# Kernel tuning notes

Hardware: AMD Instinct MI355X
Metric: run time of the kernel (lower is better)

The kernel has to match this reference:

```python
import jax, jax.numpy as jnp
import numpy as np
from jax import lax

EMB = 200   # embedding_dim (GRU hidden size)
SD = 12     # state_dim
AD = 4      # action_dim
CD = 8      # context_dim
LCD = 6     # local_context_dim
T = 100     # rollout steps
BS = 2048   # batch size
EPS = 0.01 ** 2


def _lin(x, w, b):
    # torch nn.Linear convention: y = x @ W^T + b
    return x @ w.T + b


def setup_inputs() -> dict:
    key = jax.random.key(0)
    ks = iter(jax.random.split(key, 64))

    def p(shape):
        return jax.random.normal(next(ks), shape, jnp.float32) * 0.05

    d = {}
    d["x"] = jax.random.normal(next(ks), (BS, SD), jnp.float32)
    d["u"] = jax.random.normal(next(ks), (T, BS, AD), jnp.float32)
    d["ctx_mean"] = jax.random.normal(next(ks), (BS, CD), jnp.float32)
    d["local_ctx"] = jax.random.normal(next(ks), (T, BS, LCD), jnp.float32)
    # state_embed_net: Lin(SD,200) ReLU, Lin(200,EMB) Tanh
    d["se_w1"], d["se_b1"] = p((200, SD)), p((200,))
    d["se_w2"], d["se_b2"] = p((EMB, 200)), p((EMB,))
    # action_embed_net: Lin(AD,200) ReLU, Lin(200,EMB) ReLU
    d["ae_w1"], d["ae_b1"] = p((200, AD)), p((200,))
    d["ae_w2"], d["ae_b2"] = p((EMB, 200)), p((EMB,))
    # context_embed_net: Lin(CD,200) ReLU, Lin(200,EMB) ReLU
    d["ce_w1"], d["ce_b1"] = p((200, CD)), p((200,))
    d["ce_w2"], d["ce_b2"] = p((EMB, 200)), p((EMB,))
    # local_context_embed_net: Lin(LCD,200) ReLU, Lin(200,EMB) ReLU
    d["lce_w1"], d["lce_b1"] = p((200, LCD)), p((200,))
    d["lce_w2"], d["lce_b2"] = p((EMB, 200)), p((EMB,))
    # decode_net: Lin(EMB,200) ReLU, Lin(200,SD)
    d["dec_w1"], d["dec_b1"] = p((200, EMB)), p((200,))
    d["dec_w2"], d["dec_b2"] = p((SD, 200)), p((SD,))
    # GRUCell(input=3*EMB, hidden=EMB)
    d["gru_wih"], d["gru_bih"] = p((3 * EMB, 3 * EMB)), p((3 * EMB,))
    d["gru_whh"], d["gru_bhh"] = p((3 * EMB, EMB)), p((3 * EMB,))
    # hidden_cov_net: Lin(EMB,200) ReLU, Lin(200,SD)
    d["cov_w1"], d["cov_b1"] = p((200, EMB)), p((200,))
    d["cov_w2"], d["cov_b2"] = p((SD, 200)), p((SD,))
    return d


def _forward(x, u, ctx_mean, local_ctx,
             se_w1, se_b1, se_w2, se_b2,
             ae_w1, ae_b1, ae_w2, ae_b2,
             ce_w1, ce_b1, ce_w2, ce_b2,
             lce_w1, lce_b1, lce_w2, lce_b2,
             dec_w1, dec_b1, dec_w2, dec_b2,
             gru_wih, gru_bih, gru_whh, gru_bhh,
             cov_w1, cov_b1, cov_w2, cov_b2):
    relu = jax.nn.relu
    # embeddings (vectorized over all timesteps at once)
    state_embed = jnp.tanh(_lin(relu(_lin(x, se_w1, se_b1)), se_w2, se_b2))          # [BS, EMB]
    action_embed_all = relu(_lin(relu(_lin(u, ae_w1, ae_b1)), ae_w2, ae_b2))         # [T, BS, EMB]
    ctx_embed = relu(_lin(relu(_lin(ctx_mean, ce_w1, ce_b1)), ce_w2, ce_b2))         # [BS, EMB]
    lce_all = relu(_lin(relu(_lin(local_ctx, lce_w1, lce_b1)), lce_w2, lce_b2))      # [T, BS, EMB]

    def step(h, inp):
        a, lc = inp
        gru_in = jnp.concatenate([ctx_embed, a, lc], axis=-1)   # [BS, 3*EMB]
        gi = gru_in @ gru_wih.T + gru_bih                        # [BS, 3*EMB]
        gh = h @ gru_whh.T + gru_bhh                             # [BS, 3*EMB]
        ir, iz, inn = jnp.split(gi, 3, axis=-1)
        hr, hz, hn = jnp.split(gh, 3, axis=-1)
        r = jax.nn.sigmoid(ir + hr)
        z = jax.nn.sigmoid(iz + hz)
        n = jnp.tanh(inn + r * hn)
        h_new = (1.0 - z) * n + z * h
        return h_new, h_new

    _, hs = lax.scan(step, state_embed, (action_embed_all, lce_all))
    hiddens = jnp.concatenate([state_embed[None], hs], axis=0)   # [T+1, BS, EMB]

    state_mean = _lin(relu(_lin(hiddens, dec_w1, dec_b1)), dec_w2, dec_b2)           # [T+1, BS, SD]
    cov = jax.nn.softplus(_lin(relu(_lin(hiddens, cov_w1, cov_b1)), cov_w2, cov_b2)) + EPS
    state_std = jnp.sqrt(cov)                                                        # [T+1, BS, SD]
    return state_mean, state_std


def reference(x, u, ctx_mean, local_ctx,
              se_w1, se_b1, se_w2, se_b2,
              ae_w1, ae_b1, ae_w2, ae_b2,
              ce_w1, ce_b1, ce_w2, ce_b2,
              lce_w1, lce_b1, lce_w2, lce_b2,
              dec_w1, dec_b1, dec_w2, dec_b2,
              gru_wih, gru_bih, gru_whh, gru_bhh,
              cov_w1, cov_b1, cov_w2, cov_b2):
    return _forward(x, u, ctx_mean, local_ctx,
                    se_w1, se_b1, se_w2, se_b2,
                    ae_w1, ae_b1, ae_w2, ae_b2,
                    ce_w1, ce_b1, ce_w2, ce_b2,
                    lce_w1, lce_b1, lce_w2, lce_b2,
                    dec_w1, dec_b1, dec_w2, dec_b2,
                    gru_wih, gru_bih, gru_whh, gru_bhh,
                    cov_w1, cov_b1, cov_w2, cov_b2)
```

## Files before the change

kernel.cpp:

```cpp
#include <hip/hip_runtime.h>
#include <math.h>

#define TT   100
#define BSZ  2048
#define NCH  4
#define CT   (TT/NCH)
#define CR   (CT*BSZ)
#define DR   ((TT+1)*BSZ)
#define NG   624
#define GO   208
#define EPSV 1e-4f

typedef short bfrag __attribute__((ext_vector_type(8)));
typedef float facc  __attribute__((ext_vector_type(4)));

static __device__ __forceinline__ short f2b(float x){
  union { float f; unsigned u; } c; c.f = x;
  unsigned r = (c.u + 0x7FFFu + ((c.u >> 16) & 1u)) >> 16;
  return (short)r;
}
static __device__ __forceinline__ float b2f(short s){
  union { unsigned u; float f; } c; c.u = ((unsigned)(unsigned short)s) << 16;
  return c.f;
}
static __device__ __forceinline__ facc mfma16(bfrag a, bfrag b, facc c){
  return __builtin_amdgcn_mfma_f32_16x16x32_bf16(a, b, c, 0, 0, 0);
}
static __device__ __forceinline__ float sigm(float x){ return 1.f/(1.f+__expf(-x)); }
static __device__ __forceinline__ float tanh_f(float x){
  x = fminf(fmaxf(x, -15.f), 15.f);
  float e = __expf(2.f*x);
  return (e-1.f)/(e+1.f);
}
static __device__ __forceinline__ void bar_lgkm(){
  asm volatile("s_waitcnt lgkmcnt(0)\n\ts_barrier" ::: "memory");
}

__global__ __launch_bounds__(256) void k_prep(
    const float* __restrict__ ae_w2, const float* __restrict__ lce_w2,
    const float* __restrict__ dec_w1, const float* __restrict__ cov_w1,
    const float* __restrict__ dec_w2, const float* __restrict__ cov_w2,
    const float* __restrict__ wih, const float* __restrict__ whh,
    const float* __restrict__ se_w2, const float* __restrict__ ce_w2,
    const float* __restrict__ ae_b2, const float* __restrict__ lce_b2,
    const float* __restrict__ dec_b1, const float* __restrict__ cov_b1,
    const float* __restrict__ dec_b2, const float* __restrict__ cov_b2,
    const float* __restrict__ bhh,
    const float* __restrict__ ae_w1, const float* __restrict__ ae_b1,
    const float* __restrict__ lce_w1, const float* __restrict__ lce_b1,
    short* __restrict__ aew2b, short* __restrict__ lcew2b,
    short* __restrict__ decw1b, short* __restrict__ covw1b,
    short* __restrict__ decw2b, short* __restrict__ covw2b,
    short* __restrict__ wihab, short* __restrict__ wihlb, short* __restrict__ whhb,
    float* __restrict__ sew2T, float* __restrict__ cew2T, float* __restrict__ wihcT,
    float* __restrict__ aeb2p, float* __restrict__ lceb2p,
    float* __restrict__ decb1p, float* __restrict__ covb1p,
    float* __restrict__ decb2p, float* __restrict__ covb2p,
    float* __restrict__ bhhp,
    short* __restrict__ aw1b, short* __restrict__ lw1b,
    float* __restrict__ aeb1p, float* __restrict__ lceb1p){
  int job = blockIdx.y;
  int idx = blockIdx.x*256 + threadIdx.x;
  if (job < 4){
    if (idx >= 208*224) return;
    const float* s = (job==0)?ae_w2:(job==1)?lce_w2:(job==2)?dec_w1:cov_w1;
    short* d = (job==0)?aew2b:(job==1)?lcew2b:(job==2)?decw1b:covw1b;
    int n = idx / 224, k = idx - n*224;
    d[idx] = f2b((n < 200 && k < 200) ? s[n*200 + k] : 0.f);
  } else if (job < 6){
    if (idx >= 16*224) return;
    const float* s = (job==4)?dec_w2:cov_w2;
    short* d = (job==4)?decw2b:covw2b;
    int n = idx / 224, k = idx - n*224;
    d[idx] = f2b((n < 12 && k < 200) ? s[n*200 + k] : 0.f);
  } else if (job < 8){
    if (idx >= NG*224) return;
    int colOff = (job==6) ? 200 : 400;
    short* d = (job==6)?wihab:wihlb;
    int n = idx / 224, k = idx - n*224;
    int gate = n / GO, o = n - gate*GO;
    d[idx] = f2b((o < 200 && k < 200) ? wih[(size_t)(gate*200+o)*600 + colOff + k] : 0.f);
  } else if (job == 8){
    if (idx >= NG*224) return;
    int n = idx / 224, k = idx - n*224;
    int gate = n / GO, o = n - gate*GO;
    whhb[idx] = f2b((o < 200 && k < 200) ? whh[(size_t)(gate*200+o)*200 + k] : 0.f);
  } else if (job < 11){
    if (idx >= 200*200) return;
    const float* s = (job==9)?se_w2:ce_w2;
    float* d = (job==9)?sew2T:cew2T;
    int k = idx / 200, n = idx - k*200;
    d[idx] = s[n*200 + k];
  } else if (job == 11){
    if (idx >= 200*600) return;
    int k = idx / 600, n = idx - k*600;
    wihcT[idx] = wih[(size_t)n*600 + k];
  } else if (job == 12){
    if (idx < 208)       aeb2p[idx]      = (idx < 200) ? ae_b2[idx] : 0.f;
    else if (idx < 416)  lceb2p[idx-208] = (idx-208 < 200) ? lce_b2[idx-208] : 0.f;
    else if (idx < 624)  decb1p[idx-416] = (idx-416 < 200) ? dec_b1[idx-416] : 0.f;
    else if (idx < 832)  covb1p[idx-624] = (idx-624 < 200) ? cov_b1[idx-624] : 0.f;
    else if (idx < 848)  decb2p[idx-832] = (idx-832 < 12) ? dec_b2[idx-832] : 0.f;
    else if (idx < 864)  covb2p[idx-848] = (idx-848 < 12) ? cov_b2[idx-848] : 0.f;
    else if (idx < 864+NG){
      int n = idx - 864, gate = n / GO, o = n - gate*GO;
      bhhp[n] = (o < 200) ? bhh[gate*200 + o] : 0.f;
    }
  } else {
    if (idx < 208*32){
      int n = idx >> 5, k = idx & 31;
      aw1b[idx] = f2b((n < 200 && k < 4) ? ae_w1[n*4 + k] : 0.f);
      lw1b[idx] = f2b((n < 200 && k < 6) ? lce_w1[n*6 + k] : 0.f);
    } else if (idx < 208*32 + 208){
      int n = idx - 208*32;
      aeb1p[n]  = (n < 200) ? ae_b1[n] : 0.f;
      lceb1p[n] = (n < 200) ? lce_b1[n] : 0.f;
    }
  }
}

__global__ __launch_bounds__(256) void k_zero(short* __restrict__ hidb, float* __restrict__ hcar){
  int idx = blockIdx.x*256 + threadIdx.x;
  if (idx < CR*24){
    int row = idx / 24, k = 200 + (idx - row*24);
    hidb[((size_t)BSZ + row)*224 + k] = 0;
  } else if (idx < CR*24 + BSZ*24){
    int j = idx - CR*24;
    int row = j / 24, k = 200 + (j - row*24);
    hcar[(size_t)row*224 + k] = 0.f;
  }
}

__global__ __launch_bounds__(256) void k_mlp2(const float* __restrict__ x, int Kin,
    const float* __restrict__ w1, const float* __restrict__ b1,
    const float* __restrict__ w2T, const float* __restrict__ b2,
    int act_tanh,
    float* __restrict__ outf, int outf_stride,
    short* __restrict__ outb){
  int row = blockIdx.x, t = threadIdx.x;
  __shared__ float xr[16];
  __shared__ float h1[200];
  if (t < Kin) xr[t] = x[(size_t)row*Kin + t];
  __syncthreads();
  if (t < 200){
    float a = b1[t];
    #pragma unroll 4
    for (int i = 0; i < Kin; ++i) a += xr[i] * w1[t*Kin + i];
    h1[t] = fmaxf(a, 0.f);
  }
  __syncthreads();
  if (t < 224){
    float v = 0.f;
    if (t < 200){
      float a = b2[t];
      #pragma unroll 4
      for (int k = 0; k < 200; ++k) a += h1[k] * w2T[k*200 + t];
      v = act_tanh ? tanh_f(a) : fmaxf(a, 0.f);
    }
    if (t < outf_stride) outf[(size_t)row*outf_stride + t] = v;
    if (outb) outb[(size_t)row*224 + t] = f2b(v);
  }
}

__global__ __launch_bounds__(256) void k_gictx(const float* __restrict__ ctxe,
    const float* __restrict__ wT, const float* __restrict__ bih, float* __restrict__ gic){
  int b = blockIdx.x, t = threadIdx.x;
  __shared__ float cr[200];
  if (t < 200) cr[t] = ctxe[(size_t)b*200 + t];
  __syncthreads();
  for (int n = t; n < NG; n += 256){
    int gate = n / GO, o = n - gate*GO;
    float a = 0.f;
    if (o < 200){
      int sc = gate*200 + o;
      a = bih[sc];
      #pragma unroll 4
      for (int k = 0; k < 200; ++k) a += cr[k] * wT[k*600 + sc];
    }
    gic[(size_t)b*NG + n] = a;
  }
}

__global__ __launch_bounds__(512, 2) void k_fuse(
    const float* __restrict__ u, const float* __restrict__ lc,
    const short* __restrict__ aw1b, const float* __restrict__ aeb1p,
    const short* __restrict__ lw1b, const float* __restrict__ lceb1p,
    const short* __restrict__ aw2b, const float* __restrict__ ab2p,
    const short* __restrict__ lw2b, const float* __restrict__ lb2p,
    const short* __restrict__ wihab, const short* __restrict__ wihlb,
    short* __restrict__ gibuf, int rowBase){
  __shared__ short t1[2][128][232];
  __shared__ short uB[128][40];
  __shared__ short lcB[128][40];
  int tid = threadIdx.x;
  int r0 = blockIdx.x * 128;
  for (int e = tid; e < 128*40; e += 512){
    int row = e / 40, k = e - row*40;
    size_t rg = (size_t)rowBase + r0 + row;
    uB[row][k]  = (k < 4) ? f2b(u[rg*4 + k])  : 0;
    lcB[row][k] = (k < 6) ? f2b(lc[rg*6 + k]) : 0;
  }
  for (int e = tid; e < 2*128*16; e += 512){
    int c = e & 15, row = (e >> 4) & 127, ch = e >> 11;
    t1[ch][row][208 + c] = 0;
  }
  bar_lgkm();
  int w = tid >> 6, lane = tid & 63, lm = lane & 15, lq = lane >> 4;
  int ch = w >> 2;
  int mb = (w & 3) * 2;
  {
    const short (*src)[40] = ch ? lcB : uB;
    const short* w1b = ch ? lw1b : aw1b;
    const float* b1p = ch ? lceb1p : aeb1p;
    bfrag Au0 = *reinterpret_cast<const bfrag*>(&src[mb*16 + lm][lq*8]);
    bfrag Au1 = *reinterpret_cast<const bfrag*>(&src[(mb+1)*16 + lm][lq*8]);
    for (int nt = 0; nt < 13; ++nt){
      int col = nt*16 + lm;
      bfrag Bf = *reinterpret_cast<const bfrag*>(&w1b[col*32 + lq*8]);
      facc z = {0.f,0.f,0.f,0.f};
      facc a0 = mfma16(Au0, Bf, z);
      facc a1 = mfma16(Au1, Bf, z);
      float bias = b1p[col];
      #pragma unroll
      for (int i = 0; i < 4; ++i){
        t1[ch][mb*16     + lq*4 + i][col] = f2b(fmaxf(a0[i] + bias, 0.f));
        t1[ch][(mb+1)*16 + lq*4 + i][col] = f2b(fmaxf(a1[i] + bias, 0.f));
      }
    }
  }
  bar_lgkm();
  {
    const short* w2b = ch ? lw2b : aw2b;
    const float* b2p = ch ? lb2p : ab2p;
    bfrag A0[7], A1[7];
    #pragma unroll
    for (int ks = 0; ks < 7; ++ks){
      A0[ks] = *reinterpret_cast<const bfrag*>(&t1[ch][mb*16 + lm][ks*32 + lq*8]);
      A1[ks] = *reinterpret_cast<const bfrag*>(&t1[ch][(mb+1)*16 + lm][ks*32 + lq*8]);
    }
    bfrag Bc[7], Bn[7];
    #pragma unroll
    for (int ks = 0; ks < 7; ++ks)
      Bc[ks] = *reinterpret_cast<const bfrag*>(&w2b[(size_t)lm*224 + ks*32 + lq*8]);
    for (int nt = 0; nt < 13; ++nt){
      int col = nt*16 + lm;
      if (nt < 12){
        int coln = col + 16;
        #pragma unroll
        for (int ks = 0; ks < 7; ++ks)
          Bn[ks] = *reinterpret_cast<const bfrag*>(&w2b[(size_t)coln*224 + ks*32 + lq*8]);
      }
      facc a0 = {0.f,0.f,0.f,0.f}, a1 = {0.f,0.f,0.f,0.f};
      #pragma unroll
      for (int ks = 0; ks < 7; ++ks){
        a0 = mfma16(A0[ks], Bc[ks], a0);
        a1 = mfma16(A1[ks], Bc[ks], a1);
      }
      float bias = b2p[col];
      #pragma unroll
      for (int i = 0; i < 4; ++i){
        t1[ch][mb*16     + lq*4 + i][col] = f2b(fmaxf(a0[i] + bias, 0.f));
        t1[ch][(mb+1)*16 + lq*4 + i][col] = f2b(fmaxf(a1[i] + bias, 0.f));
      }
      #pragma unroll
      for (int ks = 0; ks < 7; ++ks) Bc[ks] = Bn[ks];
    }
  }
  bar_lgkm();
  {
    int ntBase = w*5;
    int ntCnt  = (w < 7) ? 5 : 4;
    for (int gs = 0; gs < ntCnt; gs += 2){
      int gc = ntCnt - gs; if (gc > 2) gc = 2;
      bfrag Bres[2][14];
      #pragma unroll
      for (int s = 0; s < 2; ++s) if (s < gc){
        int col = (ntBase + gs + s)*16 + lm;
        #pragma unroll
        for (int ks = 0; ks < 7; ++ks){
          Bres[s][ks]   = *reinterpret_cast<const bfrag*>(&wihab[(size_t)col*224 + ks*32 + lq*8]);
          Bres[s][7+ks] = *reinterpret_cast<const bfrag*>(&wihlb[(size_t)col*224 + ks*32 + lq*8]);
        }
      }
      for (int m = 0; m < 8; ++m){
        bfrag Af[14];
        #pragma unroll
        for (int ks = 0; ks < 7; ++ks){
          Af[ks]   = *reinterpret_cast<const bfrag*>(&t1[0][m*16 + lm][ks*32 + lq*8]);
          Af[7+ks] = *reinterpret_cast<const bfrag*>(&t1[1][m*16 + lm][ks*32 + lq*8]);
        }
        #pragma unroll
        for (int s = 0; s < 2; ++s) if (s < gc){
          facc a = {0.f,0.f,0.f,0.f};
          #pragma unroll
          for (int kk = 0; kk < 14; ++kk) a = mfma16(Af[kk], Bres[s][kk], a);
          int col = (ntBase + gs + s)*16 + lm;
          #pragma unroll
          for (int i = 0; i < 4; ++i){
            int rl = m*16 + lq*4 + i;
            gibuf[((size_t)r0 + rl)*NG + col] = f2b(a[i]);
          }
        }
      }
    }
  }
}

__global__ __launch_bounds__(512, 2) void k_gru4(
    const short* __restrict__ gib, const float* __restrict__ gic,
    const float* __restrict__ hin,
    const short* __restrict__ whhb, const float* __restrict__ bhhp,
    short* __restrict__ hidb, float* __restrict__ hout){
  __shared__ float ghT[624][12];
  __shared__ short hB[2][16][232];
  int tid = threadIdx.x;
  int r0 = blockIdx.x * 8;
  int w = tid >> 6, lane = tid & 63, lm = lane & 15, lq = lane >> 4;
  int nt0 = w*5;
  int cnt = (w < 7) ? 5 : 4;
  bfrag Bg[5][7];
  float bia[5];
  #pragma unroll
  for (int s = 0; s < 5; ++s) if (s < cnt){
    int col = (nt0+s)*16 + lm;
    bia[s] = bhhp[col];
    #pragma unroll
    for (int ks = 0; ks < 7; ++ks)
      Bg[s][ks] = *reinterpret_cast<const bfrag*>(&whhb[(size_t)col*224 + ks*32 + lq*8]);
  }
  int gj = tid >> 1, grh = tid & 1;
  bool gact = (tid < 416) && (gj < 200);
  float hreg[4], gicv[3][4];
  #pragma unroll
  for (int i = 0; i < 4; ++i){
    hreg[i] = gact ? hin[(size_t)(r0 + grh*4 + i)*224 + gj] : 0.f;
    #pragma unroll
    for (int g = 0; g < 3; ++g)
      gicv[g][i] = gact ? gic[(size_t)(r0 + grh*4 + i)*NG + g*GO + gj] : 0.f;
  }
  for (int e = tid; e < 2*16*232; e += 512) (&hB[0][0][0])[e] = 0;
  __syncthreads();
  for (int e = tid; e < 8*224; e += 512){
    int row = e / 224, k = e - row*224;
    hB[0][row][k] = f2b(hin[(size_t)(r0+row)*224 + k]);
  }
  __syncthreads();
  for (int t = 0; t < CT; ++t){
    int cur = t & 1, nxt = cur ^ 1;
    float gr[4], gz[4], gn[4];
    const short* gp = gib + ((size_t)t*BSZ + r0 + grh*4)*NG + gj;
    #pragma unroll
    for (int i = 0; i < 4; ++i){
      gr[i] = gact ? b2f(gp[i*NG        ]) + gicv[0][i] : 0.f;
      gz[i] = gact ? b2f(gp[i*NG + GO   ]) + gicv[1][i] : 0.f;
      gn[i] = gact ? b2f(gp[i*NG + 2*GO ]) + gicv[2][i] : 0.f;
    }
    bfrag hf[7];
    #pragma unroll
    for (int ks = 0; ks < 7; ++ks)
      hf[ks] = *reinterpret_cast<const bfrag*>(&hB[cur][lm][ks*32 + lq*8]);
    #pragma unroll
    for (int s = 0; s < 5; ++s) if (s < cnt){
      facc a = {0.f,0.f,0.f,0.f};
      #pragma unroll
      for (int ks = 0; ks < 7; ++ks) a = mfma16(hf[ks], Bg[s][ks], a);
      if (lq < 2){
        int col = (nt0+s)*16 + lm;
        a[0] += bia[s]; a[1] += bia[s]; a[2] += bia[s]; a[3] += bia[s];
        *reinterpret_cast<facc*>(&ghT[col][lq*4]) = a;
      }
    }
    bar_lgkm();
    if (gact){
      facc R = *reinterpret_cast<facc*>(&ghT[gj][grh*4]);
      facc Z = *reinterpret_cast<facc*>(&ghT[GO + gj][grh*4]);
      facc N = *reinterpret_cast<facc*>(&ghT[2*GO + gj][grh*4]);
      short* hp = hidb + ((size_t)(t+1)*BSZ + r0 + grh*4)*224 + gj;
      #pragma unroll
      for (int i = 0; i < 4; ++i){
        float r  = sigm(gr[i] + R[i]);
        float zz = sigm(gz[i] + Z[i]);
        float n  = tanh_f(gn[i] + r*N[i]);
        float hn = (1.f - zz)*n + zz*hreg[i];
        hreg[i] = hn;
        short hb = f2b(hn);
        hB[nxt][grh*4 + i][gj] = hb;
        hp[i*224] = hb;
      }
    }
    bar_lgkm();
  }
  if (gact)
    #pragma unroll
    for (int i = 0; i < 4; ++i)
      hout[(size_t)(r0 + grh*4 + i)*224 + gj] = hreg[i];
}

__global__ __launch_bounds__(256) void k_dec(
    const short* __restrict__ hidb, int rowStart, int outBase,
    const short* __restrict__ dw1b, const float* __restrict__ db1p,
    const short* __restrict__ dw2b, const float* __restrict__ db2p,
    const short* __restrict__ cw1b, const float* __restrict__ cb1p,
    const short* __restrict__ cw2b, const float* __restrict__ cb2p,
    float* __restrict__ outMean, float* __restrict__ outStd){
  __shared__ short h1t[64][224];
  int tid = threadIdx.x;
  int r0 = rowStart + blockIdx.x * 64;
  int w = tid >> 6, lane = tid & 63, lm = lane & 15, lq = lane >> 4;
  for (int e = tid; e < 64*16; e += 256)
    h1t[e >> 4][208 + (e & 15)] = 0;
  bfrag hf[4][7];
  #pragma unroll
  for (int m = 0; m < 4; ++m)
    #pragma unroll
    for (int ks = 0; ks < 7; ++ks)
      hf[m][ks] = *reinterpret_cast<const bfrag*>(&hidb[(size_t)(r0 + m*16 + lm)*224 + ks*32 + lq*8]);
  int ntStart = (w == 0) ? 0 : 4 + 3*(w-1);
  int ntCnt   = (w == 0) ? 4 : 3;
  for (int pass = 0; pass < 2; ++pass){
    const short* w1b = pass ? cw1b : dw1b;
    const float* b1p = pass ? cb1p : db1p;
    const short* w2b = pass ? cw2b : dw2b;
    const float* b2p = pass ? cb2p : db2p;
    bar_lgkm();
    for (int nti = 0; nti < ntCnt; ++nti){
      int nt = ntStart + nti;
      int col = nt*16 + lm;
      facc z = {0.f,0.f,0.f,0.f};
      facc acc[4] = {z,z,z,z};
      #pragma unroll
      for (int ks = 0; ks < 7; ++ks){
        bfrag bf = *reinterpret_cast<const bfrag*>(&w1b[(size_t)col*224 + ks*32 + lq*8]);
        #pragma unroll
        for (int m = 0; m < 4; ++m) acc[m] = mfma16(hf[m][ks], bf, acc[m]);
      }
      float bias = b1p[col];
      #pragma unroll
      for (int m = 0; m < 4; ++m)
        #pragma unroll
        for (int i = 0; i < 4; ++i)
          h1t[m*16 + lq*4 + i][col] = f2b(fmaxf(acc[m][i] + bias, 0.f));
    }
    bar_lgkm();
    bfrag a2[7];
    #pragma unroll
    for (int ks = 0; ks < 7; ++ks)
      a2[ks] = *reinterpret_cast<const bfrag*>(&h1t[w*16 + lm][ks*32 + lq*8]);
    facc acc = {0.f,0.f,0.f,0.f};
    #pragma unroll
    for (int ks = 0; ks < 7; ++ks){
      bfrag bf = *reinterpret_cast<const bfrag*>(&w2b[(size_t)lm*224 + ks*32 + lq*8]);
      acc = mfma16(a2[ks], bf, acc);
    }
    if (lm < 12){
      float bias = b2p[lm];
      #pragma unroll
      for (int i = 0; i < 4; ++i){
        size_t rg = (size_t)outBase + r0 + w*16 + lq*4 + i;
        float v = acc[i] + bias;
        if (pass){
          float sp = (v > 15.f) ? v : log1pf(__expf(v));
          outStd[rg*12 + lm] = sqrtf(sp + EPSV);
        } else {
          outMean[rg*12 + lm] = v;
        }
      }
    }
  }
}

extern "C" void kernel_launch(void* const* d_in, const int* in_sizes, int n_in,
                              void* d_out, int out_size, void* d_ws, size_t ws_size,
                              hipStream_t stream){
  (void)in_sizes; (void)n_in; (void)out_size; (void)ws_size;
  const float* x      = (const float*)d_in[0];
  const float* u      = (const float*)d_in[1];
  const float* ctxm   = (const float*)d_in[2];
  const float* lctx   = (const float*)d_in[3];
  const float* se_w1  = (const float*)d_in[4];
  const float* se_b1  = (const float*)d_in[5];
  const float* se_w2  = (const float*)d_in[6];
  const float* se_b2  = (const float*)d_in[7];
  const float* ae_w1  = (const float*)d_in[8];
  const float* ae_b1  = (const float*)d_in[9];
  const float* ae_w2  = (const float*)d_in[10];
  const float* ae_b2  = (const float*)d_in[11];
  const float* ce_w1  = (const float*)d_in[12];
  const float* ce_b1  = (const float*)d_in[13];
  const float* ce_w2  = (const float*)d_in[14];
  const float* ce_b2  = (const float*)d_in[15];
  const float* lce_w1 = (const float*)d_in[16];
  const float* lce_b1 = (const float*)d_in[17];
  const float* lce_w2 = (const float*)d_in[18];
  const float* lce_b2 = (const float*)d_in[19];
  const float* dec_w1 = (const float*)d_in[20];
  const float* dec_b1 = (const float*)d_in[21];
  const float* dec_w2 = (const float*)d_in[22];
  const float* dec_b2 = (const float*)d_in[23];
  const float* wih    = (const float*)d_in[24];
  const float* bih    = (const float*)d_in[25];
  const float* whh    = (const float*)d_in[26];
  const float* bhh    = (const float*)d_in[27];
  const float* cov_w1 = (const float*)d_in[28];
  const float* cov_b1 = (const float*)d_in[29];
  const float* cov_w2 = (const float*)d_in[30];
  const float* cov_b2 = (const float*)d_in[31];

  char* ws = (char*)d_ws;
  size_t off = 0;
  auto alloc = [&](size_t sz) -> char* {
    char* p = ws + off; off = (off + sz + 255) & ~(size_t)255; return p;
  };
  short* aew2b  = (short*)alloc(208*224*2);
  short* lcew2b = (short*)alloc(208*224*2);
  short* decw1b = (short*)alloc(208*224*2);
  short* covw1b = (short*)alloc(208*224*2);
  short* decw2b = (short*)alloc(16*224*2);
  short* covw2b = (short*)alloc(16*224*2);
  short* wihab  = (short*)alloc((size_t)NG*224*2);
  short* wihlb  = (short*)alloc((size_t)NG*224*2);
  short* whhb   = (short*)alloc((size_t)NG*224*2);
  float* sew2T  = (float*)alloc(200*200*4);
  float* cew2T  = (float*)alloc(200*200*4);
  float* wihcT  = (float*)alloc(200*600*4);
  float* aeb2p  = (float*)alloc(208*4);
  float* lceb2p = (float*)alloc(208*4);
  float* decb1p = (float*)alloc(208*4);
  float* covb1p = (float*)alloc(208*4);
  float* decb2p = (float*)alloc(16*4);
  float* covb2p = (float*)alloc(16*4);
  float* bhhp   = (float*)alloc(NG*4);
  short* aw1b   = (short*)alloc(208*32*2);
  short* lw1b   = (short*)alloc(208*32*2);
  float* aeb1p  = (float*)alloc(208*4);
  float* lceb1p = (float*)alloc(208*4);
  float* gic    = (float*)alloc((size_t)BSZ*NG*4);
  float* h0f    = (float*)alloc((size_t)BSZ*224*4);
  float* hcar   = (float*)alloc((size_t)BSZ*224*4);
  float* ctxef  = (float*)alloc((size_t)BSZ*200*4);
  short* hidbuf = (short*)alloc((size_t)(CT+1)*BSZ*224*2);
  short* gibuf  = (short*)alloc((size_t)CR*NG*2);

  float* outMean = (float*)d_out;
  float* outStd  = outMean + (size_t)DR*12;

  k_prep<<<dim3((NG*224 + 255)/256, 14), 256, 0, stream>>>(
      ae_w2, lce_w2, dec_w1, cov_w1, dec_w2, cov_w2, wih, whh, se_w2, ce_w2,
      ae_b2, lce_b2, dec_b1, cov_b1, dec_b2, cov_b2, bhh,
      ae_w1, ae_b1, lce_w1, lce_b1,
      aew2b, lcew2b, decw1b, covw1b, decw2b, covw2b,
      wihab, wihlb, whhb, sew2T, cew2T, wihcT,
      aeb2p, lceb2p, decb1p, covb1p, decb2p, covb2p, bhhp,
      aw1b, lw1b, aeb1p, lceb1p);
  k_zero<<<(CR*24 + BSZ*24 + 255)/256, 256, 0, stream>>>(hidbuf, hcar);

  k_mlp2<<<BSZ, 256, 0, stream>>>(x,    12, se_w1, se_b1, sew2T, se_b2, 1, h0f,   224, hidbuf);
  k_mlp2<<<BSZ, 256, 0, stream>>>(ctxm,  8, ce_w1, ce_b1, cew2T, ce_b2, 0, ctxef, 200, (short*)nullptr);
  k_gictx<<<BSZ, 256, 0, stream>>>(ctxef, wihcT, bih, gic);

  for (int c = 0; c < NCH; ++c){
    k_fuse<<<CR/128, 512, 0, stream>>>(u, lctx, aw1b, aeb1p, lw1b, lceb1p,
                                       aew2b, aeb2p, lcew2b, lceb2p,
                                       wihab, wihlb, gibuf, c*CR);
    k_gru4<<<BSZ/8, 512, 0, stream>>>(gibuf, gic, (c == 0) ? h0f : hcar,
                                      whhb, bhhp, hidbuf, hcar);
    int rowStart = (c == 0) ? 0 : BSZ;
    int nRows    = (c == 0) ? (CT+1)*BSZ : CT*BSZ;
    k_dec<<<nRows/64, 256, 0, stream>>>(hidbuf, rowStart, c*CT*BSZ,
                                        decw1b, decb1p, decw2b, decb2p,
                                        covw1b, covb1p, covw2b, covb2p,
                                        outMean, outStd);
  }
}
```

Measured before the change: 1.188 ms.

## Prefetch next-step GRU gate inputs and park weight fragments in AGPRs

The GRU recurrence kernel now loads the precomputed input-gate values for step t+1 right after the barrier, while step t's gate math is still running, using a double-buffered register array. This is meant to hide global-load latency on the serial time loop. Weight fragments in the GRU and fuse kernels are pinned to accumulation registers with an empty asm constraint to ease VGPR pressure. The recurrent weight and bias buffers are padded to 640 rows so every wave handles five tiles without a branch, which adds a little wasted MFMA work.

```diff
diff --git a/kernel.cpp b/kernel.cpp
--- a/kernel.cpp
+++ b/kernel.cpp
@@ -9,6 +9,7 @@
 #define DR   ((TT+1)*BSZ)
 #define NG   624
 #define GO   208
+#define WR   640
 #define EPSV 1e-4f
 
 typedef short bfrag __attribute__((ext_vector_type(8)));
@@ -34,6 +35,9 @@
 }
 static __device__ __forceinline__ void bar_lgkm(){
   asm volatile("s_waitcnt lgkmcnt(0)\n\ts_barrier" ::: "memory");
+}
+static __device__ __forceinline__ void park(bfrag& f){
+  asm volatile("" : "+a"(f));
 }
 
 __global__ __launch_bounds__(256) void k_prep(
@@ -81,10 +85,11 @@
     int gate = n / GO, o = n - gate*GO;
     d[idx] = f2b((o < 200 && k < 200) ? wih[(size_t)(gate*200+o)*600 + colOff + k] : 0.f);
   } else if (job == 8){
-    if (idx >= NG*224) return;
+    if (idx >= WR*224) return;
     int n = idx / 224, k = idx - n*224;
     int gate = n / GO, o = n - gate*GO;
-    whhb[idx] = f2b((o < 200 && k < 200) ? whh[(size_t)(gate*200+o)*200 + k] : 0.f);
+    float v = (gate < 3 && o < 200 && k < 200) ? whh[(size_t)(gate*200+o)*200 + k] : 0.f;
+    whhb[idx] = f2b(v);
   } else if (job < 11){
     if (idx >= 200*200) return;
     const float* s = (job==9)?se_w2:ce_w2;
@@ -102,9 +107,9 @@
     else if (idx < 832)  covb1p[idx-624] = (idx-624 < 200) ? cov_b1[idx-624] : 0.f;
     else if (idx < 848)  decb2p[idx-832] = (idx-832 < 12) ? dec_b2[idx-832] : 0.f;
     else if (idx < 864)  covb2p[idx-848] = (idx-848 < 12) ? cov_b2[idx-848] : 0.f;
-    else if (idx < 864+NG){
+    else if (idx < 864+WR){
       int n = idx - 864, gate = n / GO, o = n - gate*GO;
-      bhhp[n] = (o < 200) ? bhh[gate*200 + o] : 0.f;
+      bhhp[n] = (gate < 3 && o < 200) ? bhh[gate*200 + o] : 0.f;
     }
   } else {
     if (idx < 208*32){
@@ -280,6 +285,7 @@
         for (int ks = 0; ks < 7; ++ks){
           Bres[s][ks]   = *reinterpret_cast<const bfrag*>(&wihab[(size_t)col*224 + ks*32 + lq*8]);
           Bres[s][7+ks] = *reinterpret_cast<const bfrag*>(&wihlb[(size_t)col*224 + ks*32 + lq*8]);
+          park(Bres[s][ks]); park(Bres[s][7+ks]);
         }
       }
       for (int m = 0; m < 8; ++m){
@@ -306,27 +312,28 @@
   }
 }
 
-__global__ __launch_bounds__(512, 2) void k_gru4(
+__global__ __launch_bounds__(512, 2) void k_gru5(
     const short* __restrict__ gib, const float* __restrict__ gic,
     const float* __restrict__ hin,
     const short* __restrict__ whhb, const float* __restrict__ bhhp,
     short* __restrict__ hidb, float* __restrict__ hout){
-  __shared__ float ghT[624][12];
+  __shared__ float ghT[WR][12];
   __shared__ short hB[2][16][232];
   int tid = threadIdx.x;
   int r0 = blockIdx.x * 8;
   int w = tid >> 6, lane = tid & 63, lm = lane & 15, lq = lane >> 4;
   int nt0 = w*5;
-  int cnt = (w < 7) ? 5 : 4;
   bfrag Bg[5][7];
   float bia[5];
   #pragma unroll
-  for (int s = 0; s < 5; ++s) if (s < cnt){
+  for (int s = 0; s < 5; ++s){
     int col = (nt0+s)*16 + lm;
     bia[s] = bhhp[col];
     #pragma unroll
-    for (int ks = 0; ks < 7; ++ks)
+    for (int ks = 0; ks < 7; ++ks){
       Bg[s][ks] = *reinterpret_cast<const bfrag*>(&whhb[(size_t)col*224 + ks*32 + lq*8]);
+      park(Bg[s][ks]);
+    }
   }
   int gj = tid >> 1, grh = tid & 1;
   bool gact = (tid < 416) && (gj < 200);
@@ -345,22 +352,24 @@
     hB[0][row][k] = f2b(hin[(size_t)(r0+row)*224 + k]);
   }
   __syncthreads();
+  float gv[2][3][4];
+  {
+    const short* gp = gib + ((size_t)(r0 + grh*4))*NG + gj;
+    #pragma unroll
+    for (int i = 0; i < 4; ++i){
+      gv[0][0][i] = gact ? b2f(gp[i*NG        ]) : 0.f;
+      gv[0][1][i] = gact ? b2f(gp[i*NG + GO   ]) : 0.f;
+      gv[0][2][i] = gact ? b2f(gp[i*NG + 2*GO ]) : 0.f;
+    }
+  }
   for (int t = 0; t < CT; ++t){
     int cur = t & 1, nxt = cur ^ 1;
-    float gr[4], gz[4], gn[4];
-    const short* gp = gib + ((size_t)t*BSZ + r0 + grh*4)*NG + gj;
-    #pragma unroll
-    for (int i = 0; i < 4; ++i){
-      gr[i] = gact ? b2f(gp[i*NG        ]) + gicv[0][i] : 0.f;
-      gz[i] = gact ? b2f(gp[i*NG + GO   ]) + gicv[1][i] : 0.f;
-      gn[i] = gact ? b2f(gp[i*NG + 2*GO ]) + gicv[2][i] : 0.f;
-    }
     bfrag hf[7];
     #pragma unroll
     for (int ks = 0; ks < 7; ++ks)
       hf[ks] = *reinterpret_cast<const bfrag*>(&hB[cur][lm][ks*32 + lq*8]);
     #pragma unroll
-    for (int s = 0; s < 5; ++s) if (s < cnt){
+    for (int s = 0; s < 5; ++s){
       facc a = {0.f,0.f,0.f,0.f};
       #pragma unroll
       for (int ks = 0; ks < 7; ++ks) a = mfma16(hf[ks], Bg[s][ks], a);
@@ -371,6 +380,15 @@
       }
     }
     bar_lgkm();
+    if (t + 1 < CT){
+      const short* gp = gib + ((size_t)(t+1)*BSZ + r0 + grh*4)*NG + gj;
+      #pragma unroll
+      for (int i = 0; i < 4; ++i){
+        gv[nxt][0][i] = gact ? b2f(gp[i*NG        ]) : 0.f;
+        gv[nxt][1][i] = gact ? b2f(gp[i*NG + GO   ]) : 0.f;
+        gv[nxt][2][i] = gact ? b2f(gp[i*NG + 2*GO ]) : 0.f;
+      }
+    }
     if (gact){
       facc R = *reinterpret_cast<facc*>(&ghT[gj][grh*4]);
       facc Z = *reinterpret_cast<facc*>(&ghT[GO + gj][grh*4]);
@@ -378,9 +396,9 @@
       short* hp = hidb + ((size_t)(t+1)*BSZ + r0 + grh*4)*224 + gj;
       #pragma unroll
       for (int i = 0; i < 4; ++i){
-        float r  = sigm(gr[i] + R[i]);
-        float zz = sigm(gz[i] + Z[i]);
-        float n  = tanh_f(gn[i] + r*N[i]);
+        float r  = sigm(gv[cur][0][i] + gicv[0][i] + R[i]);
+        float zz = sigm(gv[cur][1][i] + gicv[1][i] + Z[i]);
+        float n  = tanh_f(gv[cur][2][i] + gicv[2][i] + r*N[i]);
         float hn = (1.f - zz)*n + zz*hreg[i];
         hreg[i] = hn;
         short hb = f2b(hn);
@@ -519,7 +537,7 @@
   short* covw2b = (short*)alloc(16*224*2);
   short* wihab  = (short*)alloc((size_t)NG*224*2);
   short* wihlb  = (short*)alloc((size_t)NG*224*2);
-  short* whhb   = (short*)alloc((size_t)NG*224*2);
+  short* whhb   = (short*)alloc((size_t)WR*224*2);
   float* sew2T  = (float*)alloc(200*200*4);
   float* cew2T  = (float*)alloc(200*200*4);
   float* wihcT  = (float*)alloc(200*600*4);
@@ -529,7 +547,7 @@
   float* covb1p = (float*)alloc(208*4);
   float* decb2p = (float*)alloc(16*4);
   float* covb2p = (float*)alloc(16*4);
-  float* bhhp   = (float*)alloc(NG*4);
+  float* bhhp   = (float*)alloc(WR*4);
   short* aw1b   = (short*)alloc(208*32*2);
   short* lw1b   = (short*)alloc(208*32*2);
   float* aeb1p  = (float*)alloc(208*4);
@@ -544,7 +562,7 @@
   float* outMean = (float*)d_out;
   float* outStd  = outMean + (size_t)DR*12;
 
-  k_prep<<<dim3((NG*224 + 255)/256, 14), 256, 0, stream>>>(
+  k_prep<<<dim3((WR*224 + 255)/256, 14), 256, 0, stream>>>(
       ae_w2, lce_w2, dec_w1, cov_w1, dec_w2, cov_w2, wih, whh, se_w2, ce_w2,
       ae_b2, lce_b2, dec_b1, cov_b1, dec_b2, cov_b2, bhh,
       ae_w1, ae_b1, lce_w1, lce_b1,
@@ -562,7 +580,7 @@
     k_fuse<<<CR/128, 512, 0, stream>>>(u, lctx, aw1b, aeb1p, lw1b, lceb1p,
                                        aew2b, aeb2p, lcew2b, lceb2p,
                                        wihab, wihlb, gibuf, c*CR);
-    k_gru4<<<BSZ/8, 512, 0, stream>>>(gibuf, gic, (c == 0) ? h0f : hcar,
+    k_gru5<<<BSZ/8, 512, 0, stream>>>(gibuf, gic, (c == 0) ? h0f : hcar,
                                       whhb, bhhp, hidbuf, hcar);
     int rowStart = (c == 0) ? 0 : BSZ;
     int nRows    = (c == 0) ? (CT+1)*BSZ : CT*BSZ;
```

After: 1.423 ms. +19.8%, slower.
